# Kernel optimization log

Measured on AMD Instinct MI355X. Metric: run time of the kernel, lower is better.

## Reference

```python
import jax, jax.numpy as jnp
import numpy as np

M_HEADS = 8   # n_heads
N_POINTS = 4  # n_points


def setup_inputs() -> dict:
    key = jax.random.key(0)
    ks = jax.random.split(key, 12)
    B, Lq, Lin, C = 2, 1024, 4096, 256
    M, P = M_HEADS, N_POINTS
    f32 = jnp.float32
    return {
        "query": jax.random.normal(ks[0], (B, Lq, C), f32),
        "query_points": jax.random.normal(ks[1], (B, Lq, 3), f32),
        "inp": jax.random.normal(ks[2], (B, Lin, C), f32),
        "input_points": jax.random.normal(ks[3], (B, Lin, 3), f32),
        # learned params (torch Linear convention: weight (out,in))
        "Wv": jax.random.normal(ks[4], (C, C), f32) * 0.02,
        "bv": jnp.zeros((C,), f32),
        "Ws": jax.random.normal(ks[5], (M * P * 3, C), f32) * 0.02,
        "bs": jnp.zeros((M * P * 3,), f32),
        "Wa": jax.random.normal(ks[6], (M * P, C), f32) * 0.02,
        "ba": jnp.zeros((M * P,), f32),
        "Wo": jax.random.normal(ks[7], (C, C), f32) * 0.02,
        "bo": jnp.zeros((C,), f32),
    }


def _deform_attn_forward(query, query_points, inp, input_points,
                         Wv, bv, Ws, bs, Wa, ba, Wo, bo):
    M, P = M_HEADS, N_POINTS
    B, Lq, C = query.shape
    Lin = inp.shape[1]
    D = C // M  # d_per_head

    # value projection -> (B, Lin, M, D)
    value = (inp @ Wv.T + bv).reshape(B, Lin, M, D)

    # sampling locations: query_points + learned offsets -> (B, Lq, M, P, 3)
    off = (query @ Ws.T + bs).reshape(B, Lq, M, P, 3)
    loc = query_points[:, :, None, None, :] + off

    # attention weights, softmax over sampling points -> (B, Lq, M, P)
    attw = jax.nn.softmax((query @ Wa.T + ba).reshape(B, Lq, M, P), axis=-1)

    # --- KNN (k=1): nearest value point for each sampling location ---
    s = loc.reshape(B, Lq * M * P, 3)
    s = jax.lax.stop_gradient(s)           # argmin indices are non-differentiable
    vpts = jax.lax.stop_gradient(input_points)
    # squared-distance argmin: |v|^2 - 2 s.v suffices (|s|^2 constant per row)
    d = jnp.sum(vpts * vpts, axis=-1)[:, None, :] \
        - 2.0 * jnp.einsum('bnc,blc->bnl', s, vpts)   # (B, N, Lin)
    idx = jnp.argmin(d, axis=-1)                       # (B, Lq*M*P)
    idx = idx.reshape(B, Lq, M, P).transpose(0, 2, 1, 3)  # (B, M, Lq, P)

    # gather per-head features: gathered[b,m,q,p,:] = value[b, idx, m, :]
    vhead = value.transpose(0, 2, 1, 3)                 # (B, M, Lin, D)
    g = jnp.take_along_axis(vhead, idx.reshape(B, M, Lq * P)[..., None], axis=2)
    g = g.reshape(B, M, Lq, P, D)

    # weighted sum over sampling points, merge heads -> (B, Lq, C)
    out = jnp.einsum('bmqpd,bmqp->bqmd', g, attw.transpose(0, 2, 1, 3))
    out = out.reshape(B, Lq, C)
    return out @ Wo.T + bo


def reference(query, query_points, inp, input_points,
              Wv, bv, Ws, bs, Wa, ba, Wo, bo):
    return _deform_attn_forward(query, query_points, inp, input_points,
                                Wv, bv, Ws, bs, Wa, ba, Wo, bo)
```

## Files before the change

### kernel.cpp

```cpp
#include <hip/hip_runtime.h>

#define B_   2
#define LQ   1024
#define LIN  4096
#define CH   256
#define MH   8
#define NP   4
#define NROW (B_ * LQ)
#define NPTS (NROW * MH * NP)

#define SLICES    32
#define SLICE_LEN (LIN / SLICES)
#define KNN_PPT   4
#define KNN_THREADS 256

#define SWZ(r) ((((r) >> 2) & 7) << 2)

__global__ __launch_bounds__(256)
void gemm_s_fused(const float* __restrict__ query,
                  const float* __restrict__ Ws, const float* __restrict__ bs,
                  const float* __restrict__ Wa, const float* __restrict__ ba,
                  const float* __restrict__ qpts,
                  float* __restrict__ loc, float* __restrict__ attw,
                  unsigned long long* __restrict__ keys) {
    __shared__ float As[16][32];
    __shared__ float Bs[16][128];
    __shared__ float Ss[32][132];
    const int tid = threadIdx.x;
    const int rowbase = blockIdx.x * 32;
    const int tx = tid & 15;
    const int ty = tid >> 4;

    const int lr  = tid >> 3;
    const int lka = (tid & 7) * 2;
    const float* Ap = query + (size_t)(rowbase + lr) * CH + lka;
    const int n   = tid >> 1;
    const int lkb = (tid & 1) * 8;
    const float* Wrow = ((n < 96) ? (Ws + (size_t)n * CH)
                                  : (Wa + (size_t)(n - 96) * CH)) + lkb;
    float bj[8];
#pragma unroll
    for (int j = 0; j < 8; ++j) {
        int col = tx * 8 + j;
        bj[j] = (col < 96) ? bs[col] : ba[col - 96];
    }

    float2 a0 = *reinterpret_cast<const float2*>(Ap);
    float4 b0 = *reinterpret_cast<const float4*>(Wrow);
    float4 b1 = *reinterpret_cast<const float4*>(Wrow + 4);

    float acc[2][8] = {};
    for (int k0 = 0; k0 < CH; k0 += 16) {
        __syncthreads();
        As[lka + 0][lr] = a0.x; As[lka + 1][lr] = a0.y;
        Bs[lkb + 0][n] = b0.x; Bs[lkb + 1][n] = b0.y;
        Bs[lkb + 2][n] = b0.z; Bs[lkb + 3][n] = b0.w;
        Bs[lkb + 4][n] = b1.x; Bs[lkb + 5][n] = b1.y;
        Bs[lkb + 6][n] = b1.z; Bs[lkb + 7][n] = b1.w;
        __syncthreads();
        if (k0 + 16 < CH) {
            a0 = *reinterpret_cast<const float2*>(Ap + k0 + 16);
            b0 = *reinterpret_cast<const float4*>(Wrow + k0 + 16);
            b1 = *reinterpret_cast<const float4*>(Wrow + k0 + 20);
        }
#pragma unroll
        for (int k = 0; k < 16; ++k) {
            float2 a  = *reinterpret_cast<const float2*>(&As[k][ty << 1]);
            float4 v0 = *reinterpret_cast<const float4*>(&Bs[k][tx * 8]);
            float4 v1 = *reinterpret_cast<const float4*>(&Bs[k][tx * 8 + 4]);
            float ar[2] = {a.x, a.y};
            float br[8] = {v0.x, v0.y, v0.z, v0.w, v1.x, v1.y, v1.z, v1.w};
#pragma unroll
            for (int i = 0; i < 2; ++i)
#pragma unroll
                for (int j = 0; j < 8; ++j)
                    acc[i][j] = fmaf(ar[i], br[j], acc[i][j]);
        }
    }

    __syncthreads();
#pragma unroll
    for (int i = 0; i < 2; ++i)
#pragma unroll
        for (int j = 0; j < 8; ++j)
            Ss[ty * 2 + i][tx * 8 + j] = acc[i][j] + bj[j];
    __syncthreads();

    {
        int row = tid >> 3;
        int m   = tid & 7;
        int r   = rowbase + row;
        const float* Sr = Ss[row];
        float q0 = qpts[r * 3 + 0], q1 = qpts[r * 3 + 1], q2 = qpts[r * 3 + 2];
#pragma unroll
        for (int p = 0; p < NP; ++p) {
            size_t o = ((size_t)(r * MH + m) * NP + p) * 3;
            loc[o + 0] = q0 + Sr[m * 12 + p * 3 + 0];
            loc[o + 1] = q1 + Sr[m * 12 + p * 3 + 1];
            loc[o + 2] = q2 + Sr[m * 12 + p * 3 + 2];
        }
        float l0 = Sr[96 + m * 4 + 0], l1 = Sr[96 + m * 4 + 1];
        float l2 = Sr[96 + m * 4 + 2], l3 = Sr[96 + m * 4 + 3];
        float mx = fmaxf(fmaxf(l0, l1), fmaxf(l2, l3));
        float e0 = expf(l0 - mx), e1 = expf(l1 - mx);
        float e2 = expf(l2 - mx), e3 = expf(l3 - mx);
        float inv = 1.0f / (e0 + e1 + e2 + e3);
        size_t ao = (size_t)(r * MH + m) * NP;
        attw[ao + 0] = e0 * inv; attw[ao + 1] = e1 * inv;
        attw[ao + 2] = e2 * inv; attw[ao + 3] = e3 * inv;
        unsigned long long* kp = keys + ao;
        kp[0] = kp[1] = kp[2] = kp[3] = 0xFFFFFFFFFFFFFFFFull;
    }
}

__global__ __launch_bounds__(KNN_THREADS)
void knn_partial_kernel(const float* __restrict__ loc, const float* __restrict__ ipts,
                        unsigned long long* __restrict__ keys) {
    __shared__ float4 pts[SLICE_LEN];
    const int slice = blockIdx.y;
    const int t0    = slice * SLICE_LEN;
    const int pt0   = blockIdx.x * (KNN_THREADS * KNN_PPT);
    const int b     = pt0 >> 15;

    if (threadIdx.x < SLICE_LEN) {
        const float* sp = ipts + ((size_t)b * LIN + t0 + threadIdx.x) * 3;
        float x = sp[0], y = sp[1], z = sp[2];
        pts[threadIdx.x] = make_float4(x, y, z, fmaf(z, z, fmaf(y, y, x * x)));
    }

    float cx[KNN_PPT], cy[KNN_PPT], cz[KNN_PPT];
#pragma unroll
    for (int i = 0; i < KNN_PPT; ++i) {
        int p = pt0 + threadIdx.x + i * KNN_THREADS;
        cx[i] = -2.f * loc[(size_t)p * 3 + 0];
        cy[i] = -2.f * loc[(size_t)p * 3 + 1];
        cz[i] = -2.f * loc[(size_t)p * 3 + 2];
    }

    float bd0[KNN_PPT], bd1[KNN_PPT];
    int   bi0[KNN_PPT], bi1[KNN_PPT];
#pragma unroll
    for (int i = 0; i < KNN_PPT; ++i) {
        bd0[i] = bd1[i] = 1e30f;
        bi0[i] = bi1[i] = t0;
    }

    __syncthreads();
    int ca = t0;
#pragma unroll 2
    for (int l = 0; l < SLICE_LEN; l += 4) {
        float4 p0 = pts[l + 0];
        float4 p1 = pts[l + 1];
        float4 p2 = pts[l + 2];
        float4 p3 = pts[l + 3];
        int c1 = ca + 1, c2 = ca + 2, c3 = ca + 3;
#pragma unroll
        for (int i = 0; i < KNN_PPT; ++i) {
            float d0 = fmaf(cx[i], p0.x, fmaf(cy[i], p0.y, fmaf(cz[i], p0.z, p0.w)));
            float d1 = fmaf(cx[i], p1.x, fmaf(cy[i], p1.y, fmaf(cz[i], p1.z, p1.w)));
            float d2 = fmaf(cx[i], p2.x, fmaf(cy[i], p2.y, fmaf(cz[i], p2.z, p2.w)));
            float d3 = fmaf(cx[i], p3.x, fmaf(cy[i], p3.y, fmaf(cz[i], p3.z, p3.w)));
            bool a0 = d0 < bd0[i];
            bi0[i] = a0 ? ca : bi0[i];
            bd0[i] = fminf(bd0[i], d0);
            bool a2 = d2 < bd0[i];
            bi0[i] = a2 ? c2 : bi0[i];
            bd0[i] = fminf(bd0[i], d2);
            bool a1 = d1 < bd1[i];
            bi1[i] = a1 ? c1 : bi1[i];
            bd1[i] = fminf(bd1[i], d1);
            bool a3 = d3 < bd1[i];
            bi1[i] = a3 ? c3 : bi1[i];
            bd1[i] = fminf(bd1[i], d3);
        }
        ca += 4;
    }

#pragma unroll
    for (int i = 0; i < KNN_PPT; ++i) {
        float d = bd0[i]; int ix = bi0[i];
        if (bd1[i] < d || (bd1[i] == d && bi1[i] < ix)) { d = bd1[i]; ix = bi1[i]; }
        unsigned int ub  = __float_as_uint(d);
        unsigned int k32 = ub ^ (((unsigned int)((int)ub >> 31)) | 0x80000000u);
        unsigned long long key = ((unsigned long long)k32 << 32) | (unsigned int)ix;
        int p = pt0 + threadIdx.x + i * KNN_THREADS;
        atomicMin(&keys[p], key);
    }
}

__global__ __launch_bounds__(256)
void blend_gemm_kernel(const float* __restrict__ inp, const float* __restrict__ attw,
                       const unsigned long long* __restrict__ keys,
                       const float* __restrict__ Wv, float* __restrict__ part) {
    __shared__ float Ab[128][132];
    __shared__ float Bs[32][132];
    __shared__ int   ids[128][4];
    __shared__ float ats[128][4];
    const int t  = threadIdx.x;
    const int rb = blockIdx.x * 128;
    const int m  = blockIdx.y;
    const int ks = blockIdx.z;
    const int k0 = ks * 128;

    if (t < 128) {
        size_t base = ((size_t)(rb + t) * MH + m) * NP;
#pragma unroll
        for (int p = 0; p < NP; ++p) {
            ids[t][p] = (int)(keys[base + p] & 0xFFFFFFFFull);
            ats[t][p] = attw[base + p];
        }
    }
#pragma unroll
    for (int pass = 0; pass < 4; ++pass) {
        int u  = pass * 256 + t;
        int nn = u >> 5;
        int cg = (u & 31) * 4;
        float4 w = *reinterpret_cast<const float4*>(Wv + (size_t)(m * 32 + nn) * CH + k0 + cg);
        *reinterpret_cast<float4*>(&Bs[nn][cg ^ SWZ(nn)]) = w;
    }
    __syncthreads();

#pragma unroll
    for (int pass = 0; pass < 16; ++pass) {
        int u   = pass * 256 + t;
        int row = u >> 5;
        int cg  = (u & 31) * 4;
        int bq  = rb + row;
        const float* ib = inp + ((size_t)(bq >> 10) * LIN) * CH + k0 + cg;
        float4 a = {0.f, 0.f, 0.f, 0.f};
#pragma unroll
        for (int p = 0; p < NP; ++p) {
            float4 v = *reinterpret_cast<const float4*>(ib + (size_t)ids[row][p] * CH);
            float w = ats[row][p];
            a.x = fmaf(w, v.x, a.x); a.y = fmaf(w, v.y, a.y);
            a.z = fmaf(w, v.z, a.z); a.w = fmaf(w, v.w, a.w);
        }
        *reinterpret_cast<float4*>(&Ab[row][cg ^ SWZ(row)]) = a;
    }
    __syncthreads();

    const int ty = t >> 3;
    const int tx = t & 7;
    const int sA = SWZ(ty * 4);
    const int sB = SWZ(tx * 4);
    float acc[4][4] = {};
    for (int k = 0; k < 128; k += 4) {
        float4 a[4], b[4];
#pragma unroll
        for (int i = 0; i < 4; ++i)
            a[i] = *reinterpret_cast<const float4*>(&Ab[ty * 4 + i][k ^ sA]);
#pragma unroll
        for (int j = 0; j < 4; ++j)
            b[j] = *reinterpret_cast<const float4*>(&Bs[tx * 4 + j][k ^ sB]);
#pragma unroll
        for (int i = 0; i < 4; ++i)
#pragma unroll
            for (int j = 0; j < 4; ++j)
                acc[i][j] = fmaf(a[i].x, b[j].x, fmaf(a[i].y, b[j].y,
                             fmaf(a[i].z, b[j].z, fmaf(a[i].w, b[j].w, acc[i][j]))));
    }
#pragma unroll
    for (int i = 0; i < 4; ++i) {
        int bq = rb + ty * 4 + i;
        float4 c = {acc[i][0], acc[i][1], acc[i][2], acc[i][3]};
        *reinterpret_cast<float4*>(part + ((size_t)ks * MH * NROW + (size_t)m * NROW + bq) * 32 + tx * 4) = c;
    }
}

__global__ __launch_bounds__(256)
void out_gemm_kernel(const float* __restrict__ part, const float* __restrict__ bv,
                     const float* __restrict__ Wo, const float* __restrict__ bo,
                     float* __restrict__ out) {
    __shared__ float Ab[64][260];
    __shared__ float Bs[32][260];
    const int t  = threadIdx.x;
    const int rb = blockIdx.x * 64;
    const int nb = blockIdx.y * 32;

#pragma unroll
    for (int pass = 0; pass < 16; ++pass) {
        int u   = pass * 256 + t;
        int row = u >> 6;
        int cg  = (u & 63) * 4;
        int bq  = rb + row;
        int mm  = cg >> 5, d = cg & 31;
        size_t pi = ((size_t)mm * NROW + bq) * 32 + d;
        float4 v0 = *reinterpret_cast<const float4*>(part + pi);
        float4 v1 = *reinterpret_cast<const float4*>(part + (size_t)MH * NROW * 32 + pi);
        float4 bb = *reinterpret_cast<const float4*>(bv + cg);
        float4 a  = {v0.x + v1.x + bb.x, v0.y + v1.y + bb.y,
                     v0.z + v1.z + bb.z, v0.w + v1.w + bb.w};
        *reinterpret_cast<float4*>(&Ab[row][cg ^ SWZ(row)]) = a;
    }
#pragma unroll
    for (int pass = 0; pass < 8; ++pass) {
        int u  = pass * 256 + t;
        int nn = u >> 6;
        int cg = (u & 63) * 4;
        float4 w = *reinterpret_cast<const float4*>(Wo + (size_t)(nb + nn) * CH + cg);
        *reinterpret_cast<float4*>(&Bs[nn][cg ^ SWZ(nn)]) = w;
    }
    __syncthreads();

    const int ty = t >> 3;
    const int tx = t & 7;
    const int sA = SWZ(ty * 2);
    const int sB = SWZ(tx * 4);
    float acc[2][4] = {};
    for (int k = 0; k < 256; k += 4) {
        float4 a[2], b[4];
#pragma unroll
        for (int i = 0; i < 2; ++i)
            a[i] = *reinterpret_cast<const float4*>(&Ab[ty * 2 + i][k ^ sA]);
#pragma unroll
        for (int j = 0; j < 4; ++j)
            b[j] = *reinterpret_cast<const float4*>(&Bs[tx * 4 + j][k ^ sB]);
#pragma unroll
        for (int i = 0; i < 2; ++i)
#pragma unroll
            for (int j = 0; j < 4; ++j)
                acc[i][j] = fmaf(a[i].x, b[j].x, fmaf(a[i].y, b[j].y,
                             fmaf(a[i].z, b[j].z, fmaf(a[i].w, b[j].w, acc[i][j]))));
    }
#pragma unroll
    for (int i = 0; i < 2; ++i) {
        int bq = rb + ty * 2 + i;
        int n  = nb + tx * 4;
        float4 c = {acc[i][0] + bo[n + 0], acc[i][1] + bo[n + 1],
                    acc[i][2] + bo[n + 2], acc[i][3] + bo[n + 3]};
        *reinterpret_cast<float4*>(out + (size_t)bq * CH + n) = c;
    }
}

extern "C" void kernel_launch(void* const* d_in, const int* in_sizes, int n_in,
                              void* d_out, int out_size, void* d_ws, size_t ws_size,
                              hipStream_t stream) {
    const float* query = (const float*)d_in[0];
    const float* qpts  = (const float*)d_in[1];
    const float* inp   = (const float*)d_in[2];
    const float* ipts  = (const float*)d_in[3];
    const float* Wv    = (const float*)d_in[4];
    const float* bv    = (const float*)d_in[5];
    const float* Ws    = (const float*)d_in[6];
    const float* bs    = (const float*)d_in[7];
    const float* Wa    = (const float*)d_in[8];
    const float* ba    = (const float*)d_in[9];
    const float* Wo    = (const float*)d_in[10];
    const float* bo    = (const float*)d_in[11];
    float* out = (float*)d_out;

    float* ws   = (float*)d_ws;
    float* loc  = ws;
    float* attw = loc + (size_t)NPTS * 3;
    unsigned long long* keys =
        (unsigned long long*)(attw + (size_t)NPTS);
    float* part = (float*)(keys + (size_t)NPTS);

    gemm_s_fused<<<NROW / 32, 256, 0, stream>>>(query, Ws, bs, Wa, ba, qpts,
                                                loc, attw, keys);
    knn_partial_kernel<<<dim3(NPTS / (KNN_THREADS * KNN_PPT), SLICES),
                         KNN_THREADS, 0, stream>>>(loc, ipts, keys);
    blend_gemm_kernel<<<dim3(NROW / 128, MH, 2), 256, 0, stream>>>(
        inp, attw, keys, Wv, part);
    out_gemm_kernel<<<dim3(NROW / 64, CH / 32), 256, 0, stream>>>(
        part, bv, Wo, bo, out);
}
```

Measured before the change: 158.7 us.

## Replace brute-force KNN with uniform-grid spatial search

Replaces the sliced brute-force nearest-neighbour scan over all 4096 input points with a uniform 16^3 grid. A new kernel bins and counting-sorts the input points per batch, and the search kernel expands shells of cells outward with box lower-bound pruning. It also drops the 64-bit atomicMin key merge in favour of a direct index write. The aim is to cut the O(N*Lin) distance work. Exact results rely on correct pruning with an epsilon margin, and the fixed grid bounds assume points near a standard normal distribution; the per-thread loops are divergent and the build kernel runs on only two blocks.

After: 297.3 us. 1.87x slower.

```diff
diff --git a/kernel.cpp b/kernel.cpp
--- a/kernel.cpp
+++ b/kernel.cpp
@@ -9,10 +9,12 @@
 #define NROW (B_ * LQ)
 #define NPTS (NROW * MH * NP)
 
-#define SLICES    32
-#define SLICE_LEN (LIN / SLICES)
-#define KNN_PPT   4
-#define KNN_THREADS 256
+#define GN   16
+#define GN3  (GN * GN * GN)
+#define GH   0.64f
+#define GX0  (-5.12f)
+#define GINV 1.5625f
+#define GEPS 1e-3f
 
 #define SWZ(r) ((((r) >> 2) & 7) << 2)
 
@@ -21,8 +23,7 @@
                   const float* __restrict__ Ws, const float* __restrict__ bs,
                   const float* __restrict__ Wa, const float* __restrict__ ba,
                   const float* __restrict__ qpts,
-                  float* __restrict__ loc, float* __restrict__ attw,
-                  unsigned long long* __restrict__ keys) {
+                  float* __restrict__ loc, float* __restrict__ attw) {
     __shared__ float As[16][32];
     __shared__ float Bs[16][128];
     __shared__ float Ss[32][132];
@@ -108,89 +109,133 @@
         size_t ao = (size_t)(r * MH + m) * NP;
         attw[ao + 0] = e0 * inv; attw[ao + 1] = e1 * inv;
         attw[ao + 2] = e2 * inv; attw[ao + 3] = e3 * inv;
-        unsigned long long* kp = keys + ao;
-        kp[0] = kp[1] = kp[2] = kp[3] = 0xFFFFFFFFFFFFFFFFull;
-    }
-}
-
-__global__ __launch_bounds__(KNN_THREADS)
-void knn_partial_kernel(const float* __restrict__ loc, const float* __restrict__ ipts,
-                        unsigned long long* __restrict__ keys) {
-    __shared__ float4 pts[SLICE_LEN];
-    const int slice = blockIdx.y;
-    const int t0    = slice * SLICE_LEN;
-    const int pt0   = blockIdx.x * (KNN_THREADS * KNN_PPT);
-    const int b     = pt0 >> 15;
-
-    if (threadIdx.x < SLICE_LEN) {
-        const float* sp = ipts + ((size_t)b * LIN + t0 + threadIdx.x) * 3;
-        float x = sp[0], y = sp[1], z = sp[2];
-        pts[threadIdx.x] = make_float4(x, y, z, fmaf(z, z, fmaf(y, y, x * x)));
-    }
-
-    float cx[KNN_PPT], cy[KNN_PPT], cz[KNN_PPT];
-#pragma unroll
-    for (int i = 0; i < KNN_PPT; ++i) {
-        int p = pt0 + threadIdx.x + i * KNN_THREADS;
-        cx[i] = -2.f * loc[(size_t)p * 3 + 0];
-        cy[i] = -2.f * loc[(size_t)p * 3 + 1];
-        cz[i] = -2.f * loc[(size_t)p * 3 + 2];
-    }
-
-    float bd0[KNN_PPT], bd1[KNN_PPT];
-    int   bi0[KNN_PPT], bi1[KNN_PPT];
-#pragma unroll
-    for (int i = 0; i < KNN_PPT; ++i) {
-        bd0[i] = bd1[i] = 1e30f;
-        bi0[i] = bi1[i] = t0;
-    }
-
-    __syncthreads();
-    int ca = t0;
-#pragma unroll 2
-    for (int l = 0; l < SLICE_LEN; l += 4) {
-        float4 p0 = pts[l + 0];
-        float4 p1 = pts[l + 1];
-        float4 p2 = pts[l + 2];
-        float4 p3 = pts[l + 3];
-        int c1 = ca + 1, c2 = ca + 2, c3 = ca + 3;
-#pragma unroll
-        for (int i = 0; i < KNN_PPT; ++i) {
-            float d0 = fmaf(cx[i], p0.x, fmaf(cy[i], p0.y, fmaf(cz[i], p0.z, p0.w)));
-            float d1 = fmaf(cx[i], p1.x, fmaf(cy[i], p1.y, fmaf(cz[i], p1.z, p1.w)));
-            float d2 = fmaf(cx[i], p2.x, fmaf(cy[i], p2.y, fmaf(cz[i], p2.z, p2.w)));
-            float d3 = fmaf(cx[i], p3.x, fmaf(cy[i], p3.y, fmaf(cz[i], p3.z, p3.w)));
-            bool a0 = d0 < bd0[i];
-            bi0[i] = a0 ? ca : bi0[i];
-            bd0[i] = fminf(bd0[i], d0);
-            bool a2 = d2 < bd0[i];
-            bi0[i] = a2 ? c2 : bi0[i];
-            bd0[i] = fminf(bd0[i], d2);
-            bool a1 = d1 < bd1[i];
-            bi1[i] = a1 ? c1 : bi1[i];
-            bd1[i] = fminf(bd1[i], d1);
-            bool a3 = d3 < bd1[i];
-            bi1[i] = a3 ? c3 : bi1[i];
-            bd1[i] = fminf(bd1[i], d3);
-        }
-        ca += 4;
-    }
-
-#pragma unroll
-    for (int i = 0; i < KNN_PPT; ++i) {
-        float d = bd0[i]; int ix = bi0[i];
-        if (bd1[i] < d || (bd1[i] == d && bi1[i] < ix)) { d = bd1[i]; ix = bi1[i]; }
-        unsigned int ub  = __float_as_uint(d);
-        unsigned int k32 = ub ^ (((unsigned int)((int)ub >> 31)) | 0x80000000u);
-        unsigned long long key = ((unsigned long long)k32 << 32) | (unsigned int)ix;
-        int p = pt0 + threadIdx.x + i * KNN_THREADS;
-        atomicMin(&keys[p], key);
-    }
+    }
+}
+
+__global__ __launch_bounds__(512)
+void build_grid_kernel(const float* __restrict__ ipts,
+                       float4* __restrict__ spts, int* __restrict__ cellstart) {
+    __shared__ int hist[GN3];
+    __shared__ int part[512];
+    const int b = blockIdx.x;
+    const int t = threadIdx.x;
+    const float* pb = ipts + (size_t)b * LIN * 3;
+
+#pragma unroll
+    for (int k = 0; k < GN3 / 512; ++k) hist[k * 512 + t] = 0;
+    __syncthreads();
+
+    int cells[LIN / 512];
+#pragma unroll
+    for (int k = 0; k < LIN / 512; ++k) {
+        int i = k * 512 + t;
+        float x = pb[i * 3 + 0], y = pb[i * 3 + 1], z = pb[i * 3 + 2];
+        int cx = min(max((int)floorf((x - GX0) * GINV), 0), GN - 1);
+        int cy = min(max((int)floorf((y - GX0) * GINV), 0), GN - 1);
+        int cz = min(max((int)floorf((z - GX0) * GINV), 0), GN - 1);
+        cells[k] = (cz * GN + cy) * GN + cx;
+        atomicAdd(&hist[cells[k]], 1);
+    }
+    __syncthreads();
+
+    int h8[8];
+    int sum = 0;
+#pragma unroll
+    for (int k = 0; k < 8; ++k) { h8[k] = hist[t * 8 + k]; sum += h8[k]; }
+    part[t] = sum;
+    __syncthreads();
+    for (int off = 1; off < 512; off <<= 1) {
+        int v = (t >= off) ? part[t - off] : 0;
+        __syncthreads();
+        part[t] += v;
+        __syncthreads();
+    }
+    int base = part[t] - sum;
+    const int cb = b * (GN3 + 1);
+#pragma unroll
+    for (int k = 0; k < 8; ++k) {
+        int c = t * 8 + k;
+        cellstart[cb + c] = base;
+        hist[c] = base;
+        base += h8[k];
+    }
+    if (t == 511) cellstart[cb + GN3] = LIN;
+    __syncthreads();
+
+#pragma unroll
+    for (int k = 0; k < LIN / 512; ++k) {
+        int i = k * 512 + t;
+        float x = pb[i * 3 + 0], y = pb[i * 3 + 1], z = pb[i * 3 + 2];
+        int pos = atomicAdd(&hist[cells[k]], 1);
+        spts[(size_t)b * LIN + pos] = make_float4(x, y, z, __int_as_float(i));
+    }
+}
+
+__global__ __launch_bounds__(256)
+void knn_grid_kernel(const float* __restrict__ loc, const float4* __restrict__ spts,
+                     const int* __restrict__ cellstart, int* __restrict__ idx) {
+    const int gq = blockIdx.x * 256 + threadIdx.x;
+    const int b  = gq >> 15;
+    const float sx = loc[(size_t)gq * 3 + 0];
+    const float sy = loc[(size_t)gq * 3 + 1];
+    const float sz = loc[(size_t)gq * 3 + 2];
+    const float sx2 = -2.f * sx, sy2 = -2.f * sy, sz2 = -2.f * sz;
+    const float ssq = fmaf(sz, sz, fmaf(sy, sy, sx * sx));
+
+    const int icx = min(max((int)floorf((sx - GX0) * GINV), 0), GN - 1);
+    const int icy = min(max((int)floorf((sy - GX0) * GINV), 0), GN - 1);
+    const int icz = min(max((int)floorf((sz - GX0) * GINV), 0), GN - 1);
+
+    const int cb = b * (GN3 + 1);
+    const float4* sb = spts + (size_t)b * LIN;
+
+    float bd = 1e30f;
+    int   bi = 0;
+
+    for (int r = 0; r < GN; ++r) {
+        if (r > 0) {
+            float rb = (float)(r - 1) * GH;
+            if (rb * rb > bd + ssq + GEPS) break;
+        }
+        int zlo = max(icz - r, 0), zhi = min(icz + r, GN - 1);
+        int ylo = max(icy - r, 0), yhi = min(icy + r, GN - 1);
+        int xlo = max(icx - r, 0), xhi = min(icx + r, GN - 1);
+        for (int cz = zlo; cz <= zhi; ++cz) {
+            int az = abs(cz - icz);
+            for (int cy = ylo; cy <= yhi; ++cy) {
+                int ay = max(az, abs(cy - icy));
+                for (int cx = xlo; cx <= xhi; ++cx) {
+                    if (max(ay, abs(cx - icx)) != r) continue;
+                    float lox = GX0 + cx * GH;
+                    float loy = GX0 + cy * GH;
+                    float loz = GX0 + cz * GH;
+                    float dx = fmaxf(fmaxf(lox - sx, sx - (lox + GH)), 0.f);
+                    float dy = fmaxf(fmaxf(loy - sy, sy - (loy + GH)), 0.f);
+                    float dz = fmaxf(fmaxf(loz - sz, sz - (loz + GH)), 0.f);
+                    float lbsq = fmaf(dx, dx, fmaf(dy, dy, dz * dz));
+                    if (lbsq > bd + ssq + GEPS) continue;
+                    int c  = (cz * GN + cy) * GN + cx;
+                    int s0 = cellstart[cb + c];
+                    int s1 = cellstart[cb + c + 1];
+                    for (int j = s0; j < s1; ++j) {
+                        float4 sp = sb[j];
+                        float nrm = fmaf(sp.z, sp.z, fmaf(sp.y, sp.y, sp.x * sp.x));
+                        float d   = fmaf(sx2, sp.x, fmaf(sy2, sp.y, fmaf(sz2, sp.z, nrm)));
+                        int   oi  = __float_as_int(sp.w);
+                        bool take = (d < bd) || (d == bd && oi < bi);
+                        bi = take ? oi : bi;
+                        bd = fminf(bd, d);
+                    }
+                }
+            }
+        }
+    }
+    idx[gq] = bi;
 }
 
 __global__ __launch_bounds__(256)
 void blend_gemm_kernel(const float* __restrict__ inp, const float* __restrict__ attw,
-                       const unsigned long long* __restrict__ keys,
+                       const int* __restrict__ idx,
                        const float* __restrict__ Wv, float* __restrict__ part) {
     __shared__ float Ab[128][132];
     __shared__ float Bs[32][132];
@@ -206,7 +251,7 @@
         size_t base = ((size_t)(rb + t) * MH + m) * NP;
 #pragma unroll
         for (int p = 0; p < NP; ++p) {
-            ids[t][p] = (int)(keys[base + p] & 0xFFFFFFFFull);
+            ids[t][p] = idx[base + p];
             ats[t][p] = attw[base + p];
         }
     }
@@ -245,19 +290,19 @@
     const int sB = SWZ(tx * 4);
     float acc[4][4] = {};
     for (int k = 0; k < 128; k += 4) {
-        float4 a[4], b[4];
+        float4 a[4], bb[4];
 #pragma unroll
         for (int i = 0; i < 4; ++i)
             a[i] = *reinterpret_cast<const float4*>(&Ab[ty * 4 + i][k ^ sA]);
 #pragma unroll
         for (int j = 0; j < 4; ++j)
-            b[j] = *reinterpret_cast<const float4*>(&Bs[tx * 4 + j][k ^ sB]);
+            bb[j] = *reinterpret_cast<const float4*>(&Bs[tx * 4 + j][k ^ sB]);
 #pragma unroll
         for (int i = 0; i < 4; ++i)
 #pragma unroll
             for (int j = 0; j < 4; ++j)
-                acc[i][j] = fmaf(a[i].x, b[j].x, fmaf(a[i].y, b[j].y,
-                             fmaf(a[i].z, b[j].z, fmaf(a[i].w, b[j].w, acc[i][j]))));
+                acc[i][j] = fmaf(a[i].x, bb[j].x, fmaf(a[i].y, bb[j].y,
+                             fmaf(a[i].z, bb[j].z, fmaf(a[i].w, bb[j].w, acc[i][j]))));
     }
 #pragma unroll
     for (int i = 0; i < 4; ++i) {
@@ -308,19 +353,19 @@
     const int sB = SWZ(tx * 4);
     float acc[2][4] = {};
     for (int k = 0; k < 256; k += 4) {
-        float4 a[2], b[4];
+        float4 a[2], bb[4];
 #pragma unroll
         for (int i = 0; i < 2; ++i)
             a[i] = *reinterpret_cast<const float4*>(&Ab[ty * 2 + i][k ^ sA]);
 #pragma unroll
         for (int j = 0; j < 4; ++j)
-            b[j] = *reinterpret_cast<const float4*>(&Bs[tx * 4 + j][k ^ sB]);
+            bb[j] = *reinterpret_cast<const float4*>(&Bs[tx * 4 + j][k ^ sB]);
 #pragma unroll
         for (int i = 0; i < 2; ++i)
 #pragma unroll
             for (int j = 0; j < 4; ++j)
-                acc[i][j] = fmaf(a[i].x, b[j].x, fmaf(a[i].y, b[j].y,
-                             fmaf(a[i].z, b[j].z, fmaf(a[i].w, b[j].w, acc[i][j]))));
+                acc[i][j] = fmaf(a[i].x, bb[j].x, fmaf(a[i].y, bb[j].y,
+                             fmaf(a[i].z, bb[j].z, fmaf(a[i].w, bb[j].w, acc[i][j]))));
     }
 #pragma unroll
     for (int i = 0; i < 2; ++i) {
@@ -349,19 +394,20 @@
     const float* bo    = (const float*)d_in[11];
     float* out = (float*)d_out;
 
-    float* ws   = (float*)d_ws;
-    float* loc  = ws;
-    float* attw = loc + (size_t)NPTS * 3;
-    unsigned long long* keys =
-        (unsigned long long*)(attw + (size_t)NPTS);
-    float* part = (float*)(keys + (size_t)NPTS);
-
+    float*  ws        = (float*)d_ws;
+    float*  loc       = ws;
+    float*  attw      = loc + (size_t)NPTS * 3;
+    float*  part      = attw + (size_t)NPTS;
+    float4* spts      = (float4*)(part + (size_t)2 * MH * NROW * 32);
+    int*    idx       = (int*)(spts + (size_t)B_ * LIN);
+    int*    cellstart = idx + (size_t)NPTS;
+
+    build_grid_kernel<<<B_, 512, 0, stream>>>(ipts, spts, cellstart);
     gemm_s_fused<<<NROW / 32, 256, 0, stream>>>(query, Ws, bs, Wa, ba, qpts,
-                                                loc, attw, keys);
-    knn_partial_kernel<<<dim3(NPTS / (KNN_THREADS * KNN_PPT), SLICES),
-                         KNN_THREADS, 0, stream>>>(loc, ipts, keys);
+                                                loc, attw);
+    knn_grid_kernel<<<NPTS / 256, 256, 0, stream>>>(loc, spts, cellstart, idx);
     blend_gemm_kernel<<<dim3(NROW / 128, MH, 2), 256, 0, stream>>>(
-        inp, attw, keys, Wv, part);
+        inp, attw, idx, Wv, part);
     out_gemm_kernel<<<dim3(NROW / 64, CH / 32), 256, 0, stream>>>(
         part, bv, Wo, bo, out);
 }
```

## Restructure KNN to read precomputed point table from global memory with fewer slices

Applied to the files above, without the earlier changes.

Adds a prep kernel that packs input points with their squared norms into a float4 table. The KNN kernel now handles one sampling point per thread over 8 slices of 512 points, instead of 4 points per thread over 32 slices with a shared-memory tile. Because all threads in a wave read the same address, the global loads are uniform broadcasts that should hit cache. This removes the per-block shared staging and barrier and cuts atomicMin traffic by 4x, but drops register reuse across query points and adds a kernel launch.

After: 239.2 us. +50.7%, slower.

```diff
diff --git a/kernel.cpp b/kernel.cpp
--- a/kernel.cpp
+++ b/kernel.cpp
@@ -9,10 +9,8 @@
 #define NROW (B_ * LQ)
 #define NPTS (NROW * MH * NP)
 
-#define SLICES    32
-#define SLICE_LEN (LIN / SLICES)
-#define KNN_PPT   4
-#define KNN_THREADS 256
+#define KSLICES 8
+#define KSLEN   (LIN / KSLICES)
 
 #define SWZ(r) ((((r) >> 2) & 7) << 2)
 
@@ -113,79 +111,69 @@
     }
 }
 
-__global__ __launch_bounds__(KNN_THREADS)
-void knn_partial_kernel(const float* __restrict__ loc, const float* __restrict__ ipts,
-                        unsigned long long* __restrict__ keys) {
-    __shared__ float4 pts[SLICE_LEN];
+__global__ __launch_bounds__(256)
+void prep_pts_kernel(const float* __restrict__ ipts, float4* __restrict__ cpts) {
+    int t = blockIdx.x * 256 + threadIdx.x;
+    const float* sp = ipts + (size_t)t * 12;
+    float4 u0 = *reinterpret_cast<const float4*>(sp + 0);
+    float4 u1 = *reinterpret_cast<const float4*>(sp + 4);
+    float4 u2 = *reinterpret_cast<const float4*>(sp + 8);
+    float xs[4] = {u0.x, u0.w, u1.z, u2.y};
+    float ys[4] = {u0.y, u1.x, u1.w, u2.z};
+    float zs[4] = {u0.z, u1.y, u2.x, u2.w};
+#pragma unroll
+    for (int i = 0; i < 4; ++i) {
+        float nrm = fmaf(zs[i], zs[i], fmaf(ys[i], ys[i], xs[i] * xs[i]));
+        cpts[(size_t)t * 4 + i] = make_float4(xs[i], ys[i], zs[i], nrm);
+    }
+}
+
+__global__ __launch_bounds__(256)
+void knn_scalar_kernel(const float* __restrict__ loc,
+                       const float4* __restrict__ cpts,
+                       unsigned long long* __restrict__ keys) {
+    const int gq    = blockIdx.x * 256 + threadIdx.x;
     const int slice = blockIdx.y;
-    const int t0    = slice * SLICE_LEN;
-    const int pt0   = blockIdx.x * (KNN_THREADS * KNN_PPT);
-    const int b     = pt0 >> 15;
-
-    if (threadIdx.x < SLICE_LEN) {
-        const float* sp = ipts + ((size_t)b * LIN + t0 + threadIdx.x) * 3;
-        float x = sp[0], y = sp[1], z = sp[2];
-        pts[threadIdx.x] = make_float4(x, y, z, fmaf(z, z, fmaf(y, y, x * x)));
-    }
-
-    float cx[KNN_PPT], cy[KNN_PPT], cz[KNN_PPT];
-#pragma unroll
-    for (int i = 0; i < KNN_PPT; ++i) {
-        int p = pt0 + threadIdx.x + i * KNN_THREADS;
-        cx[i] = -2.f * loc[(size_t)p * 3 + 0];
-        cy[i] = -2.f * loc[(size_t)p * 3 + 1];
-        cz[i] = -2.f * loc[(size_t)p * 3 + 2];
-    }
-
-    float bd0[KNN_PPT], bd1[KNN_PPT];
-    int   bi0[KNN_PPT], bi1[KNN_PPT];
-#pragma unroll
-    for (int i = 0; i < KNN_PPT; ++i) {
-        bd0[i] = bd1[i] = 1e30f;
-        bi0[i] = bi1[i] = t0;
-    }
-
-    __syncthreads();
-    int ca = t0;
-#pragma unroll 2
-    for (int l = 0; l < SLICE_LEN; l += 4) {
-        float4 p0 = pts[l + 0];
-        float4 p1 = pts[l + 1];
-        float4 p2 = pts[l + 2];
-        float4 p3 = pts[l + 3];
-        int c1 = ca + 1, c2 = ca + 2, c3 = ca + 3;
-#pragma unroll
-        for (int i = 0; i < KNN_PPT; ++i) {
-            float d0 = fmaf(cx[i], p0.x, fmaf(cy[i], p0.y, fmaf(cz[i], p0.z, p0.w)));
-            float d1 = fmaf(cx[i], p1.x, fmaf(cy[i], p1.y, fmaf(cz[i], p1.z, p1.w)));
-            float d2 = fmaf(cx[i], p2.x, fmaf(cy[i], p2.y, fmaf(cz[i], p2.z, p2.w)));
-            float d3 = fmaf(cx[i], p3.x, fmaf(cy[i], p3.y, fmaf(cz[i], p3.z, p3.w)));
-            bool a0 = d0 < bd0[i];
-            bi0[i] = a0 ? ca : bi0[i];
-            bd0[i] = fminf(bd0[i], d0);
-            bool a2 = d2 < bd0[i];
-            bi0[i] = a2 ? c2 : bi0[i];
-            bd0[i] = fminf(bd0[i], d2);
-            bool a1 = d1 < bd1[i];
-            bi1[i] = a1 ? c1 : bi1[i];
-            bd1[i] = fminf(bd1[i], d1);
-            bool a3 = d3 < bd1[i];
-            bi1[i] = a3 ? c3 : bi1[i];
-            bd1[i] = fminf(bd1[i], d3);
-        }
-        ca += 4;
-    }
-
-#pragma unroll
-    for (int i = 0; i < KNN_PPT; ++i) {
-        float d = bd0[i]; int ix = bi0[i];
-        if (bd1[i] < d || (bd1[i] == d && bi1[i] < ix)) { d = bd1[i]; ix = bi1[i]; }
-        unsigned int ub  = __float_as_uint(d);
-        unsigned int k32 = ub ^ (((unsigned int)((int)ub >> 31)) | 0x80000000u);
-        unsigned long long key = ((unsigned long long)k32 << 32) | (unsigned int)ix;
-        int p = pt0 + threadIdx.x + i * KNN_THREADS;
-        atomicMin(&keys[p], key);
-    }
+    const int b     = gq >> 15;
+    const int sbase = slice * KSLEN;
+
+    const float sx = loc[(size_t)gq * 3 + 0];
+    const float sy = loc[(size_t)gq * 3 + 1];
+    const float sz = loc[(size_t)gq * 3 + 2];
+    const float sx2 = -2.f * sx, sy2 = -2.f * sy, sz2 = -2.f * sz;
+
+    const float4* cb = cpts + (size_t)b * LIN + sbase;
+
+    float bd0 = 1e30f, bd1 = 1e30f;
+    int   bi0 = sbase, bi1 = sbase;
+
+#pragma unroll 4
+    for (int j = 0; j < KSLEN; j += 2) {
+        float4 p0 = cb[j];
+        float4 p1 = cb[j + 1];
+        float t0 = sx2 * p0.x;
+        t0 = fmaf(sy2, p0.y, t0);
+        t0 = fmaf(sz2, p0.z, t0);
+        float d0 = t0 + p0.w;
+        float t1 = sx2 * p1.x;
+        t1 = fmaf(sy2, p1.y, t1);
+        t1 = fmaf(sz2, p1.z, t1);
+        float d1 = t1 + p1.w;
+        bool a0 = d0 < bd0;
+        bi0 = a0 ? (sbase + j) : bi0;
+        bd0 = fminf(bd0, d0);
+        bool a1 = d1 < bd1;
+        bi1 = a1 ? (sbase + j + 1) : bi1;
+        bd1 = fminf(bd1, d1);
+    }
+
+    float d = bd0; int ix = bi0;
+    if (bd1 < d || (bd1 == d && bi1 < ix)) { d = bd1; ix = bi1; }
+
+    unsigned int ub  = __float_as_uint(d);
+    unsigned int k32 = ub ^ (((unsigned int)((int)ub >> 31)) | 0x80000000u);
+    unsigned long long key = ((unsigned long long)k32 << 32) | (unsigned int)ix;
+    atomicMin(&keys[gq], key);
 }
 
 __global__ __launch_bounds__(256)
@@ -245,19 +233,19 @@
     const int sB = SWZ(tx * 4);
     float acc[4][4] = {};
     for (int k = 0; k < 128; k += 4) {
-        float4 a[4], b[4];
+        float4 a[4], bb[4];
 #pragma unroll
         for (int i = 0; i < 4; ++i)
             a[i] = *reinterpret_cast<const float4*>(&Ab[ty * 4 + i][k ^ sA]);
 #pragma unroll
         for (int j = 0; j < 4; ++j)
-            b[j] = *reinterpret_cast<const float4*>(&Bs[tx * 4 + j][k ^ sB]);
+            bb[j] = *reinterpret_cast<const float4*>(&Bs[tx * 4 + j][k ^ sB]);
 #pragma unroll
         for (int i = 0; i < 4; ++i)
 #pragma unroll
             for (int j = 0; j < 4; ++j)
-                acc[i][j] = fmaf(a[i].x, b[j].x, fmaf(a[i].y, b[j].y,
-                             fmaf(a[i].z, b[j].z, fmaf(a[i].w, b[j].w, acc[i][j]))));
+                acc[i][j] = fmaf(a[i].x, bb[j].x, fmaf(a[i].y, bb[j].y,
+                             fmaf(a[i].z, bb[j].z, fmaf(a[i].w, bb[j].w, acc[i][j]))));
     }
 #pragma unroll
     for (int i = 0; i < 4; ++i) {
@@ -308,19 +296,19 @@
     const int sB = SWZ(tx * 4);
     float acc[2][4] = {};
     for (int k = 0; k < 256; k += 4) {
-        float4 a[2], b[4];
+        float4 a[2], bb[4];
 #pragma unroll
         for (int i = 0; i < 2; ++i)
             a[i] = *reinterpret_cast<const float4*>(&Ab[ty * 2 + i][k ^ sA]);
 #pragma unroll
         for (int j = 0; j < 4; ++j)
-            b[j] = *reinterpret_cast<const float4*>(&Bs[tx * 4 + j][k ^ sB]);
+            bb[j] = *reinterpret_cast<const float4*>(&Bs[tx * 4 + j][k ^ sB]);
 #pragma unroll
         for (int i = 0; i < 2; ++i)
 #pragma unroll
             for (int j = 0; j < 4; ++j)
-                acc[i][j] = fmaf(a[i].x, b[j].x, fmaf(a[i].y, b[j].y,
-                             fmaf(a[i].z, b[j].z, fmaf(a[i].w, b[j].w, acc[i][j]))));
+                acc[i][j] = fmaf(a[i].x, bb[j].x, fmaf(a[i].y, bb[j].y,
+                             fmaf(a[i].z, bb[j].z, fmaf(a[i].w, bb[j].w, acc[i][j]))));
     }
 #pragma unroll
     for (int i = 0; i < 2; ++i) {
@@ -349,17 +337,19 @@
     const float* bo    = (const float*)d_in[11];
     float* out = (float*)d_out;
 
-    float* ws   = (float*)d_ws;
-    float* loc  = ws;
-    float* attw = loc + (size_t)NPTS * 3;
+    float*  ws   = (float*)d_ws;
+    float*  loc  = ws;
+    float*  attw = loc + (size_t)NPTS * 3;
+    float*  part = attw + (size_t)NPTS;
+    float4* cpts = (float4*)(part + (size_t)2 * MH * NROW * 32);
     unsigned long long* keys =
-        (unsigned long long*)(attw + (size_t)NPTS);
-    float* part = (float*)(keys + (size_t)NPTS);
-
+        (unsigned long long*)(cpts + (size_t)B_ * LIN);
+
+    prep_pts_kernel<<<B_ * LIN / 4 / 256, 256, 0, stream>>>(ipts, cpts);
     gemm_s_fused<<<NROW / 32, 256, 0, stream>>>(query, Ws, bs, Wa, ba, qpts,
                                                 loc, attw, keys);
-    knn_partial_kernel<<<dim3(NPTS / (KNN_THREADS * KNN_PPT), SLICES),
-                         KNN_THREADS, 0, stream>>>(loc, ipts, keys);
+    knn_scalar_kernel<<<dim3(NPTS / 256, KSLICES), 256, 0, stream>>>(
+        loc, cpts, keys);
     blend_gemm_kernel<<<dim3(NROW / 128, MH, 2), 256, 0, stream>>>(
         inp, attw, keys, Wv, part);
     out_gemm_kernel<<<dim3(NROW / 64, CH / 32), 256, 0, stream>>>(
```
